# Kernel tuning notes

Hardware: AMD Instinct MI355X
Metric: run time of the kernel (lower is better)

Reference implementation:

```python
import jax, jax.numpy as jnp
import numpy as np

B, C, H, W = 4, 64, 64, 64
DK, DV = 64, 64


def _conv1x1(x, w, b):
    # x: [B,C,H,W], w: [O,C], b: [O] -> [B,O,H,W]
    return jnp.einsum('bchw,oc->bohw', x, w) + b[None, :, None, None]


def _ordered_mask(N, ordering, dtype):
    mask = jnp.tril(jnp.ones((N, N), dtype=dtype))
    if ordering == 1:
        return mask
    elif ordering == 2:
        return jnp.flip(mask, 1)
    elif ordering == 3:
        return jnp.rot90(mask, 1)
    elif ordering == 4:
        return jnp.flip(jnp.rot90(mask, 1), 0)
    elif ordering == 5:
        return jnp.rot90(mask, 2)
    elif ordering == 6:
        return jnp.flip(jnp.rot90(mask, 2), 1)
    elif ordering == 7:
        return jnp.rot90(mask, 3)
    elif ordering == 8:
        return jnp.flip(jnp.rot90(mask, 3), 1)
    return None


def setup_inputs() -> dict:
    key = jax.random.key(0)
    ks = jax.random.split(key, 9)
    s = 0.02
    return {
        'x': jax.random.normal(ks[0], (B, C, H, W), dtype=jnp.float32),
        'Wq': jax.random.normal(ks[1], (DK, C), dtype=jnp.float32) * s,
        'bq': jnp.zeros((DK,), dtype=jnp.float32),
        'Wk': jax.random.normal(ks[2], (DK, C), dtype=jnp.float32) * s,
        'bk': jnp.zeros((DK,), dtype=jnp.float32),
        'Wv': jax.random.normal(ks[3], (DV, C), dtype=jnp.float32) * s,
        'bv': jnp.zeros((DV,), dtype=jnp.float32),
        'Wo': jax.random.normal(ks[4], (DV, DV + C), dtype=jnp.float32) * s,
        'bo': jnp.zeros((DV,), dtype=jnp.float32),
        'ordering': 1,
    }


def reference(x, Wq, bq, Wk, bk, Wv, bv, Wo, bo, ordering):
    b, c, h, w = x.shape
    N = h * w
    dk, dv = Wq.shape[0], Wv.shape[0]
    Q = _conv1x1(x, Wq, bq).reshape(b, dk, N)  # [B,dk,N]
    K = _conv1x1(x, Wk, bk).reshape(b, dk, N)  # [B,dk,N]
    V = _conv1x1(x, Wv, bv).reshape(b, dv, N)  # [B,dv,N]
    logits = jnp.einsum('bdn,bdm->bnm', Q, K)  # [B,N,N] (no 1/sqrt(dk) scaling, matching source)
    weights = jax.nn.softmax(logits, axis=-1)
    m = _ordered_mask(N, ordering, x.dtype)
    if m is not None:
        weights = weights * m  # post-softmax multiplicative mask
    o = jnp.einsum('bnm,bdm->bdn', weights, V).reshape(b, dv, h, w)
    oc = jnp.concatenate([o, x], axis=1)  # [B,dv+C,H,W]
    return _conv1x1(oc, Wo, bo)
```

## Files before the change

kernel.cpp:

```cpp
#include <hip/hip_runtime.h>

typedef __attribute__((ext_vector_type(8))) short short8;
typedef __attribute__((ext_vector_type(4))) short short4v;
typedef __attribute__((ext_vector_type(4))) float f32x4;
typedef __attribute__((ext_vector_type(16))) float f32x16;
typedef __attribute__((ext_vector_type(4))) unsigned int uint4v;
typedef __attribute__((ext_vector_type(2))) unsigned int uint2v;
typedef unsigned short us;
typedef unsigned int u32;

#define NB 4
#define NC 64
#define NN 4096
#define ND 64
#define LOG2E 1.44269504088896340736f

static __device__ __forceinline__ us f2bf(float x) {
    u32 u = __builtin_bit_cast(u32, x);
    u += 0x7FFFu + ((u >> 16) & 1u);
    return (us)(u >> 16);
}

static __device__ __forceinline__ float bf2f(us v) {
    u32 u = ((u32)v) << 16;
    return __builtin_bit_cast(float, u);
}

static __device__ __forceinline__ u32 cvtpk(float a, float b) {
    u32 r;
    asm("v_cvt_pk_bf16_f32 %0, %1, %2" : "=v"(r) : "v"(a), "v"(b));
    return r;
}

static __device__ __forceinline__ short8 comb(short4v a, short4v b) {
    short8 r;
    r[0] = a[0]; r[1] = a[1]; r[2] = a[2]; r[3] = a[3];
    r[4] = b[0]; r[5] = b[1]; r[6] = b[2]; r[7] = b[3];
    return r;
}

static __device__ __forceinline__ void async_copy16(void* lds, const void* g) {
    __builtin_amdgcn_global_load_lds(
        (const __attribute__((address_space(1))) u32*)g,
        (__attribute__((address_space(3))) u32*)lds, 16, 0, 0);
}

static __device__ __forceinline__ int swz8(int row) {
    return (row & 7) ^ ((row >> 3) & 3);
}

__global__ void cvt_kernel(const float* __restrict__ Wo,
                           const float* __restrict__ Wq,
                           const float* __restrict__ Wk,
                           const float* __restrict__ Wv,
                           us* __restrict__ Wob, us* __restrict__ Wqb,
                           us* __restrict__ Wkb, us* __restrict__ Wvb) {
    int i = blockIdx.x * 256 + threadIdx.x;
    if (i < 8192) Wob[i] = f2bf(Wo[i]);
    else if (i < 12288) Wqb[i - 8192] = f2bf(Wq[i - 8192] * LOG2E);
    else if (i < 16384) Wkb[i - 12288] = f2bf(Wk[i - 12288]);
    else if (i < 20480) Wvb[i - 16384] = f2bf(Wv[i - 16384]);
}

__global__ __launch_bounds__(256) void proj_kernel(
    const float* __restrict__ x,
    const us* __restrict__ Wqb, const float* __restrict__ bq,
    const us* __restrict__ Wkb, const float* __restrict__ bk,
    const us* __restrict__ Wvb, const float* __restrict__ bv,
    us* __restrict__ Qt, us* __restrict__ Kt,
    us* __restrict__ Vm, us* __restrict__ Xbt)
{
    __shared__ float xs[64][64];
    __shared__ __align__(16) us xT[64][64];
    const int t = threadIdx.x;
    const int bid = blockIdx.x;
    const int role = bid & 1;
    const int v = bid >> 1;
    const int b = v >> 6;
    const int n0 = (v & 63) << 6;
    const float* xb = x + (size_t)b * NC * NN + n0;
    #pragma unroll
    for (int i = 0; i < 4; ++i) {
        int s = t + i * 256;
        int c = s >> 4, col = (s & 15) << 2;
        *(f32x4*)&xs[c][col] = *(const f32x4*)&xb[(size_t)c * NN + col];
    }
    __syncthreads();
    {
        int n = t & 63, cg = t >> 6;
        int c0 = cg << 4;
        u32 pk[8];
        #pragma unroll
        for (int j = 0; j < 8; ++j) {
            float a0 = xs[c0 + 2 * j][n], a1 = xs[c0 + 2 * j + 1][n];
            pk[j] = (u32)f2bf(a0) | ((u32)f2bf(a1) << 16);
        }
        int b0 = (cg * 2) ^ (n & 7), b1 = (cg * 2 + 1) ^ (n & 7);
        *(uint4v*)&xT[n][b0 * 8] = (uint4v){pk[0], pk[1], pk[2], pk[3]};
        *(uint4v*)&xT[n][b1 * 8] = (uint4v){pk[4], pk[5], pk[6], pk[7]};
        if (role == 1) {
            us* dst = Xbt + (size_t)(b * NN + n0 + n) * ND + c0;
            *(uint4v*)dst       = (uint4v){pk[0], pk[1], pk[2], pk[3]};
            *(uint4v*)(dst + 8) = (uint4v){pk[4], pk[5], pk[6], pk[7]};
        }
    }
    __syncthreads();
    const int w = t >> 6, l = t & 63, h = l >> 4, ln = l & 15;
    const int row = w * 16 + ln;
    short8 xq0 = *(const short8*)&xT[row][((h ^ (row & 7)) << 3)];
    short8 xq1 = *(const short8*)&xT[row][(((4 + h) ^ (row & 7)) << 3)];

    if (role == 0) {
        #pragma unroll
        for (int p = 0; p < 2; ++p) {
            const us* Wb = p ? Wkb : Wqb;
            const float* bias = p ? bk : bq;
            const float sc = p ? 1.0f : LOG2E;
            us* outp = p ? Kt : Qt;
            #pragma unroll
            for (int di = 0; di < 4; ++di) {
                const int d = di * 16 + ln;
                const us* wrb = Wb + (size_t)d * 64;
                short8 a0 = *(const short8*)(wrb + h * 8);
                short8 a1 = *(const short8*)(wrb + 32 + h * 8);
                f32x4 acc = *(const f32x4*)(bias + di * 16 + h * 4);
                acc *= sc;
                acc = __builtin_amdgcn_mfma_f32_16x16x32_bf16(a0, xq0, acc, 0, 0, 0);
                acc = __builtin_amdgcn_mfma_f32_16x16x32_bf16(a1, xq1, acc, 0, 0, 0);
                u32 lo = (u32)f2bf(acc[0]) | ((u32)f2bf(acc[1]) << 16);
                u32 hi2 = (u32)f2bf(acc[2]) | ((u32)f2bf(acc[3]) << 16);
                *(uint2v*)(outp + (size_t)(b * NN + n0 + row) * ND + di * 16 + h * 4) = (uint2v){lo, hi2};
            }
        }
    } else {
        #pragma unroll
        for (int di = 0; di < 4; ++di) {
            const int d = di * 16 + ln;
            const us* wrb = Wvb + (size_t)d * 64;
            short8 a0 = *(const short8*)(wrb + h * 8);
            short8 a1 = *(const short8*)(wrb + 32 + h * 8);
            f32x4 acc = *(const f32x4*)(bv + di * 16 + h * 4);
            acc = __builtin_amdgcn_mfma_f32_16x16x32_bf16(a0, xq0, acc, 0, 0, 0);
            acc = __builtin_amdgcn_mfma_f32_16x16x32_bf16(a1, xq1, acc, 0, 0, 0);
            us* vp = Vm + (size_t)(b * ND + di * 16 + h * 4) * NN + n0 + row;
            vp[0] = f2bf(acc[0]); vp[NN] = f2bf(acc[1]);
            vp[2 * NN] = f2bf(acc[2]); vp[3 * NN] = f2bf(acc[3]);
        }
    }
}

static __device__ __forceinline__ void mask_bounds32(int pt, int n032, int ng,
    int& lo_n, int& hi_n, int& lo_min, int& lo_max, int& hi_min, int& hi_max)
{
    if (pt == 0)      { lo_n = 0;           hi_n = ng;          lo_min = 0;              lo_max = 0;             hi_min = n032;           hi_max = n032 + 31; }
    else if (pt == 1) { lo_n = NN - 1 - ng; hi_n = NN - 1;      lo_min = NN - 32 - n032; lo_max = NN - 1 - n032; hi_min = NN - 1;         hi_max = NN - 1; }
    else if (pt == 2) { lo_n = ng;          hi_n = NN - 1;      lo_min = n032;           lo_max = n032 + 31;     hi_min = NN - 1;         hi_max = NN - 1; }
    else if (pt == 3) { lo_n = 0;           hi_n = NN - 1 - ng; lo_min = 0;              lo_max = 0;             hi_min = NN - 32 - n032; hi_max = NN - 1 - n032; }
    else              { lo_n = 0;           hi_n = NN - 1;      lo_min = 0;              lo_max = 0;             hi_min = NN - 1;         hi_max = NN - 1; }
}

__global__ __launch_bounds__(256, 4) void attn_kernel(
    const us* __restrict__ Qt, const us* __restrict__ Kt,
    const us* __restrict__ Vm,
    const int* __restrict__ ordp,
    us* __restrict__ Opb, float* __restrict__ Lb)
{
    __shared__ __align__(16) us Kl[2][64 * 64];
    __shared__ __align__(16) us Vl[2][64 * 64];

    const int tid = threadIdx.x;
    const int w = tid >> 6, l = tid & 63;
    const int hi = l >> 5, ln = l & 31;
    const int nh = w & 1, mh = (w >> 1) & 1;
    const int bid = blockIdx.x;
    const int vid = (bid & 7) * 128 + (bid >> 3);
    const int b = vid >> 8;
    const int ms = (vid >> 6) & 3;
    const int n0 = (vid & 63) << 6;
    const int mbase = ms << 10;
    const int n032 = n0 + nh * 32;
    const int ng = n032 + ln;

    const int ord = ordp[0];
    int pt = 4;
    if (ord == 1) pt = 0;
    else if (ord == 2 || ord == 3) pt = 1;
    else if (ord == 4 || ord == 5 || ord == 8) pt = 2;
    else if (ord == 6 || ord == 7) pt = 3;
    int lo_n, hi_n, lo_min, lo_max, hi_min, hi_max;
    mask_bounds32(pt, n032, ng, lo_n, hi_n, lo_min, lo_max, hi_min, hi_max);

    int vlo = 0, vhi = NN - 1;
    if (pt == 0)      { vhi = n0 + 63; }
    else if (pt == 1) { vlo = NN - 64 - n0; }
    else if (pt == 2) { vlo = n0; }
    else if (pt == 3) { vhi = NN - 1 - n0; }

    const us* kb = Kt + (size_t)b * NN * ND;
    const us* vb = Vm + (size_t)b * ND * NN;
    const us* qrow = Qt + (size_t)(b * NN + n032 + ln) * ND;
    short8 qf0 = *(const short8*)(qrow + 0 * 16 + hi * 8);
    short8 qf1 = *(const short8*)(qrow + 1 * 16 + hi * 8);
    short8 qf2 = *(const short8*)(qrow + 2 * 16 + hi * 8);
    short8 qf3 = *(const short8*)(qrow + 3 * 16 + hi * 8);

    f32x16 O0, O1, Z;
    #pragma unroll
    for (int i = 0; i < 16; ++i) { O0[i] = 0.f; O1[i] = 0.f; Z[i] = 0.f; }
    float Lp = 0.f;

    auto stage = [&](int buf, int t) {
        const int m_base = mbase + t * 64;
        if (w < 2) {
            #pragma unroll
            for (int r = 0; r < 4; ++r) {
                const int rl = w * 32 + r * 8 + (l >> 3);
                const int blk = l & 7;
                const us* src = kb + (size_t)(m_base + rl) * ND + ((blk ^ swz8(rl)) << 3);
                async_copy16(&Kl[buf][(w * 32 + r * 8) * 64], src);
            }
        } else {
            if (m_base + 63 < vlo || m_base > vhi) return;
            #pragma unroll
            for (int r = 0; r < 4; ++r) {
                const int rl = (w - 2) * 32 + r * 8 + (l >> 3);
                const int blk = l & 7;
                const us* src = vb + (size_t)rl * NN + m_base + ((blk ^ swz8(rl)) << 3);
                async_copy16(&Vl[buf][((w - 2) * 32 + r * 8) * 64], src);
            }
        }
    };

    stage(0, 0);
    for (int t = 0; t < 16; ++t) {
        if (t < 15) {
            stage((t + 1) & 1, t + 1);
            asm volatile("s_waitcnt vmcnt(4)" ::: "memory");
        } else {
            asm volatile("s_waitcnt vmcnt(0)" ::: "memory");
        }
        __builtin_amdgcn_s_barrier();
        __builtin_amdgcn_sched_barrier(0);

        const us* KT = Kl[t & 1];
        const us* VT = Vl[t & 1];
        const int m0s = mbase + t * 64 + mh * 32;
        const bool skip = (m0s + 31 < lo_min) || (m0s > hi_max);
        const bool full = (m0s >= lo_max) && (m0s + 31 <= hi_min);

        __builtin_amdgcn_s_setprio(1);
        {
            const int row = mh * 32 + ln;
            const int rs = swz8(row);
            short8 a0 = *(const short8*)&KT[row * 64 + (((0 + hi) ^ rs) << 3)];
            short8 a1 = *(const short8*)&KT[row * 64 + (((2 + hi) ^ rs) << 3)];
            short8 a2 = *(const short8*)&KT[row * 64 + (((4 + hi) ^ rs) << 3)];
            short8 a3 = *(const short8*)&KT[row * 64 + (((6 + hi) ^ rs) << 3)];
            f32x16 st = __builtin_amdgcn_mfma_f32_32x32x16_bf16(a0, qf0, Z, 0, 0, 0);
            st = __builtin_amdgcn_mfma_f32_32x32x16_bf16(a1, qf1, st, 0, 0, 0);
            st = __builtin_amdgcn_mfma_f32_32x32x16_bf16(a2, qf2, st, 0, 0, 0);
            st = __builtin_amdgcn_mfma_f32_32x32x16_bf16(a3, qf3, st, 0, 0, 0);

            float p[16];
            float lp0 = 0.f, lp1 = 0.f;
            #pragma unroll
            for (int r = 0; r < 16; ++r) {
                p[r] = __builtin_amdgcn_exp2f(st[r]);
                if (r & 1) lp1 += p[r]; else lp0 += p[r];
            }
            Lp += lp0 + lp1;
            if (!skip) {
                if (!full) {
                    #pragma unroll
                    for (int r = 0; r < 16; ++r) {
                        const int mg = m0s + (r & 3) + 8 * (r >> 2) + 4 * hi;
                        if (mg < lo_n || mg > hi_n) p[r] = 0.f;
                    }
                }
                #pragma unroll
                for (int c16 = 0; c16 < 2; ++c16) {
                    uint4v pw;
                    pw[0] = cvtpk(p[c16 * 8 + 0], p[c16 * 8 + 1]);
                    pw[1] = cvtpk(p[c16 * 8 + 2], p[c16 * 8 + 3]);
                    pw[2] = cvtpk(p[c16 * 8 + 4], p[c16 * 8 + 5]);
                    pw[3] = cvtpk(p[c16 * 8 + 6], p[c16 * 8 + 7]);
                    short8 pb = __builtin_bit_cast(short8, pw);
                    const int blkA = mh * 4 + c16 * 2;
                    {
                        const int rv = ln, rvs = swz8(rv);
                        short4v va  = *(const short4v*)&VT[rv * 64 + ((blkA ^ rvs) << 3) + hi * 4];
                        short4v vb2 = *(const short4v*)&VT[rv * 64 + (((blkA + 1) ^ rvs) << 3) + hi * 4];
                        O0 = __builtin_amdgcn_mfma_f32_32x32x16_bf16(comb(va, vb2), pb, O0, 0, 0, 0);
                    }
                    {
                        const int rv = 32 + ln, rvs = swz8(rv);
                        short4v va  = *(const short4v*)&VT[rv * 64 + ((blkA ^ rvs) << 3) + hi * 4];
                        short4v vb2 = *(const short4v*)&VT[rv * 64 + (((blkA + 1) ^ rvs) << 3) + hi * 4];
                        O1 = __builtin_amdgcn_mfma_f32_32x32x16_bf16(comb(va, vb2), pb, O1, 0, 0, 0);
                    }
                }
            }
        }
        __builtin_amdgcn_s_setprio(0);
        __builtin_amdgcn_sched_barrier(0);
        __builtin_amdgcn_s_barrier();
    }

    float Lw = Lp + __shfl_xor(Lp, 32);

    float* cO = (float*)&Kl[0][0];
    float* cL = (float*)&Vl[0][0];
    if (mh == 1) {
        float* dsto = cO + nh * 2048 + ln * 64;
        #pragma unroll
        for (int rq = 0; rq < 4; ++rq) {
            f32x4 s0, s1;
            #pragma unroll
            for (int j = 0; j < 4; ++j) { s0[j] = O0[rq * 4 + j]; s1[j] = O1[rq * 4 + j]; }
            *(f32x4*)&dsto[rq * 8 + hi * 4] = s0;
            *(f32x4*)&dsto[32 + rq * 8 + hi * 4] = s1;
        }
        if (hi == 0) cL[nh * 32 + ln] = Lw;
    }
    __syncthreads();
    if (mh == 1) return;

    const float gL = Lw + cL[nh * 32 + ln];
    const float* sp = cO + nh * 2048 + ln * 64;
    f32x16 On0 = O0, On1 = O1;
    #pragma unroll
    for (int rq = 0; rq < 4; ++rq) {
        f32x4 a = *(const f32x4*)&sp[rq * 8 + hi * 4];
        f32x4 c = *(const f32x4*)&sp[32 + rq * 8 + hi * 4];
        #pragma unroll
        for (int j = 0; j < 4; ++j) { On0[rq * 4 + j] += a[j]; On1[rq * 4 + j] += c[j]; }
    }

    us* opb = Opb + ((size_t)(ms * NB + b) * 64) * NN;
    #pragma unroll
    for (int r = 0; r < 16; ++r) {
        const int d0 = (r & 3) + 8 * (r >> 2) + 4 * hi;
        opb[(size_t)d0 * NN + n032 + ln] = f2bf(On0[r]);
        opb[(size_t)(d0 + 32) * NN + n032 + ln] = f2bf(On1[r]);
    }
    if (hi == 0) Lb[(size_t)(ms * NB + b) * NN + n032 + ln] = gL;
}

__global__ __launch_bounds__(256) void combine_kernel(
    const us* __restrict__ Opb, const float* __restrict__ Lb,
    const us* __restrict__ Xbt, const us* __restrict__ Wob,
    const float* __restrict__ bo, float* __restrict__ out)
{
    const int t = threadIdx.x;
    const int w = t >> 6, l = t & 63, hi = l >> 5, ln = l & 31;
    const int gw = blockIdx.x * 4 + w;
    const int b = gw >> 7;
    const int n032 = (gw & 127) << 5;
    const int q = n032 + ln;

    f32x16 On0, On1;
    #pragma unroll
    for (int r = 0; r < 16; ++r) {
        const int d0 = (r & 3) + 8 * (r >> 2) + 4 * hi;
        float s0 = 0.f, s1 = 0.f;
        #pragma unroll
        for (int i = 0; i < 4; ++i) {
            const us* opb = Opb + ((size_t)(i * NB + b) * 64) * NN;
            s0 += bf2f(opb[(size_t)d0 * NN + q]);
            s1 += bf2f(opb[(size_t)(d0 + 32) * NN + q]);
        }
        On0[r] = s0; On1[r] = s1;
    }
    float gL = 0.f;
    #pragma unroll
    for (int i = 0; i < 4; ++i) gL += Lb[(size_t)(i * NB + b) * NN + q];
    const float rl2 = 1.0f / gL;
    #pragma unroll
    for (int i = 0; i < 16; ++i) { On0[i] *= rl2; On1[i] *= rl2; }

    short8 Bf[8];
    {
        uint4v w0, w1, w2, w3;
        w0[0] = cvtpk(On0[0], On0[1]);   w0[1] = cvtpk(On0[2], On0[3]);
        w0[2] = cvtpk(On0[4], On0[5]);   w0[3] = cvtpk(On0[6], On0[7]);
        w1[0] = cvtpk(On0[8], On0[9]);   w1[1] = cvtpk(On0[10], On0[11]);
        w1[2] = cvtpk(On0[12], On0[13]); w1[3] = cvtpk(On0[14], On0[15]);
        w2[0] = cvtpk(On1[0], On1[1]);   w2[1] = cvtpk(On1[2], On1[3]);
        w2[2] = cvtpk(On1[4], On1[5]);   w2[3] = cvtpk(On1[6], On1[7]);
        w3[0] = cvtpk(On1[8], On1[9]);   w3[1] = cvtpk(On1[10], On1[11]);
        w3[2] = cvtpk(On1[12], On1[13]); w3[3] = cvtpk(On1[14], On1[15]);
        Bf[0] = __builtin_bit_cast(short8, w0);
        Bf[1] = __builtin_bit_cast(short8, w1);
        Bf[2] = __builtin_bit_cast(short8, w2);
        Bf[3] = __builtin_bit_cast(short8, w3);
    }
    const us* xrow = Xbt + (size_t)(b * NN + q) * ND;
    #pragma unroll
    for (int c4 = 0; c4 < 4; ++c4)
        Bf[4 + c4] = comb(*(const short4v*)(xrow + c4 * 16 + hi * 4),
                          *(const short4v*)(xrow + c4 * 16 + hi * 4 + 8));

    f32x16 acc0, acc1;
    #pragma unroll
    for (int rq = 0; rq < 4; ++rq) {
        f32x4 b0 = *(const f32x4*)&bo[rq * 8 + hi * 4];
        f32x4 b1 = *(const f32x4*)&bo[32 + rq * 8 + hi * 4];
        #pragma unroll
        for (int j = 0; j < 4; ++j) { acc0[rq * 4 + j] = b0[j]; acc1[rq * 4 + j] = b1[j]; }
    }
    const us* wr0 = Wob + (size_t)ln * 128;
    const us* wr1 = Wob + (size_t)(32 + ln) * 128;
    #pragma unroll
    for (int kc = 0; kc < 8; ++kc) {
        short8 wf0 = comb(*(const short4v*)(wr0 + kc * 16 + hi * 4),
                          *(const short4v*)(wr0 + kc * 16 + hi * 4 + 8));
        short8 wf1 = comb(*(const short4v*)(wr1 + kc * 16 + hi * 4),
                          *(const short4v*)(wr1 + kc * 16 + hi * 4 + 8));
        acc0 = __builtin_amdgcn_mfma_f32_32x32x16_bf16(wf0, Bf[kc], acc0, 0, 0, 0);
        acc1 = __builtin_amdgcn_mfma_f32_32x32x16_bf16(wf1, Bf[kc], acc1, 0, 0, 0);
    }
    #pragma unroll
    for (int r = 0; r < 16; ++r) {
        const int od = (r & 3) + 8 * (r >> 2) + 4 * hi;
        out[((size_t)b * 64 + od) * NN + q] = acc0[r];
        out[((size_t)b * 64 + 32 + od) * NN + q] = acc1[r];
    }
}

extern "C" void kernel_launch(void* const* d_in, const int* in_sizes, int n_in,
                              void* d_out, int out_size, void* d_ws, size_t ws_size,
                              hipStream_t stream) {
    (void)in_sizes; (void)n_in; (void)out_size; (void)ws_size;
    const float* x  = (const float*)d_in[0];
    const float* Wq = (const float*)d_in[1];
    const float* bq = (const float*)d_in[2];
    const float* Wk = (const float*)d_in[3];
    const float* bk = (const float*)d_in[4];
    const float* Wv = (const float*)d_in[5];
    const float* bv = (const float*)d_in[6];
    const float* Wo = (const float*)d_in[7];
    const float* bo = (const float*)d_in[8];
    const int* ord  = (const int*)d_in[9];
    float* out = (float*)d_out;

    us* Qt  = (us*)d_ws;
    us* Kt  = Qt  + (size_t)NB * NN * ND;
    us* Vm  = Kt  + (size_t)NB * NN * ND;
    us* Xbt = Vm  + (size_t)NB * NN * ND;
    us* Wob = Xbt + (size_t)NB * NN * ND;
    us* Opb = Wob + ND * (ND + NC);
    float* Lb = (float*)(Opb + (size_t)4 * NB * 64 * NN);
    us* Wqb = (us*)(Lb + (size_t)4 * NB * NN);
    us* Wkb = Wqb + 4096;
    us* Wvb = Wkb + 4096;

    cvt_kernel<<<dim3(80), dim3(256), 0, stream>>>(Wo, Wq, Wk, Wv, Wob, Wqb, Wkb, Wvb);
    proj_kernel<<<dim3(NB * 64 * 2), dim3(256), 0, stream>>>(
        x, Wqb, bq, Wkb, bk, Wvb, bv, Qt, Kt, Vm, Xbt);
    attn_kernel<<<dim3(1024), dim3(256), 0, stream>>>(Qt, Kt, Vm, ord, Opb, Lb);
    combine_kernel<<<dim3(128), dim3(256), 0, stream>>>(Opb, Lb, Xbt, Wob, bo, out);
}
```

Measured before the change: 56.50 us.

## Triple-buffer K/V staging, pack partial outputs as bf16 pairs, shrink combine blocks

The attention kernel moves from double to triple LDS buffering, prefetching two tiles ahead and dropping the trailing per-iteration barrier. It also removes the V-load skip for masked tiles and lowers the occupancy hint from 4 to 3 blocks per SM. Partial outputs are now written as packed bf16 pairs (u32) for wider stores and loads, and the combine kernel runs 512 single-wave blocks instead of 128 four-wave blocks. The aim is to hide global-load latency and cut store and load transaction counts, at the cost of more LDS, lower occupancy and extra V traffic on masked tiles.

```diff
diff --git a/kernel.cpp b/kernel.cpp
--- a/kernel.cpp
+++ b/kernel.cpp
@@ -159,14 +159,14 @@
     else              { lo_n = 0;           hi_n = NN - 1;      lo_min = 0;              lo_max = 0;             hi_min = NN - 1;         hi_max = NN - 1; }
 }
 
-__global__ __launch_bounds__(256, 4) void attn_kernel(
+__global__ __launch_bounds__(256, 3) void attn_kernel(
     const us* __restrict__ Qt, const us* __restrict__ Kt,
     const us* __restrict__ Vm,
     const int* __restrict__ ordp,
-    us* __restrict__ Opb, float* __restrict__ Lb)
+    u32* __restrict__ Opk, float* __restrict__ Lb)
 {
-    __shared__ __align__(16) us Kl[2][64 * 64];
-    __shared__ __align__(16) us Vl[2][64 * 64];
+    __shared__ __align__(16) us Kl[3][64 * 64];
+    __shared__ __align__(16) us Vl[3][64 * 64];
 
     const int tid = threadIdx.x;
     const int w = tid >> 6, l = tid & 63;
@@ -190,12 +190,6 @@
     int lo_n, hi_n, lo_min, lo_max, hi_min, hi_max;
     mask_bounds32(pt, n032, ng, lo_n, hi_n, lo_min, lo_max, hi_min, hi_max);
 
-    int vlo = 0, vhi = NN - 1;
-    if (pt == 0)      { vhi = n0 + 63; }
-    else if (pt == 1) { vlo = NN - 64 - n0; }
-    else if (pt == 2) { vlo = n0; }
-    else if (pt == 3) { vhi = NN - 1 - n0; }
-
     const us* kb = Kt + (size_t)b * NN * ND;
     const us* vb = Vm + (size_t)b * ND * NN;
     const us* qrow = Qt + (size_t)(b * NN + n032 + ln) * ND;
@@ -220,7 +214,6 @@
                 async_copy16(&Kl[buf][(w * 32 + r * 8) * 64], src);
             }
         } else {
-            if (m_base + 63 < vlo || m_base > vhi) return;
             #pragma unroll
             for (int r = 0; r < 4; ++r) {
                 const int rl = (w - 2) * 32 + r * 8 + (l >> 3);
@@ -232,9 +225,12 @@
     };
 
     stage(0, 0);
+    stage(1, 1);
     for (int t = 0; t < 16; ++t) {
-        if (t < 15) {
-            stage((t + 1) & 1, t + 1);
+        if (t < 14) {
+            stage((t + 2) % 3, t + 2);
+            asm volatile("s_waitcnt vmcnt(8)" ::: "memory");
+        } else if (t == 14) {
             asm volatile("s_waitcnt vmcnt(4)" ::: "memory");
         } else {
             asm volatile("s_waitcnt vmcnt(0)" ::: "memory");
@@ -242,8 +238,9 @@
         __builtin_amdgcn_s_barrier();
         __builtin_amdgcn_sched_barrier(0);
 
-        const us* KT = Kl[t & 1];
-        const us* VT = Vl[t & 1];
+        const int bc = t % 3;
+        const us* KT = Kl[bc];
+        const us* VT = Vl[bc];
         const int m0s = mbase + t * 64 + mh * 32;
         const bool skip = (m0s + 31 < lo_min) || (m0s > hi_max);
         const bool full = (m0s >= lo_max) && (m0s + 31 <= hi_min);
@@ -303,9 +300,9 @@
         }
         __builtin_amdgcn_s_setprio(0);
         __builtin_amdgcn_sched_barrier(0);
-        __builtin_amdgcn_s_barrier();
-    }
-
+    }
+
+    __syncthreads();
     float Lw = Lp + __shfl_xor(Lp, 32);
 
     float* cO = (float*)&Kl[0][0];
@@ -336,40 +333,43 @@
         for (int j = 0; j < 4; ++j) { On0[rq * 4 + j] += a[j]; On1[rq * 4 + j] += c[j]; }
     }
 
-    us* opb = Opb + ((size_t)(ms * NB + b) * 64) * NN;
-    #pragma unroll
-    for (int r = 0; r < 16; ++r) {
-        const int d0 = (r & 3) + 8 * (r >> 2) + 4 * hi;
-        opb[(size_t)d0 * NN + n032 + ln] = f2bf(On0[r]);
-        opb[(size_t)(d0 + 32) * NN + n032 + ln] = f2bf(On1[r]);
-    }
-    if (hi == 0) Lb[(size_t)(ms * NB + b) * NN + n032 + ln] = gL;
-}
-
-__global__ __launch_bounds__(256) void combine_kernel(
-    const us* __restrict__ Opb, const float* __restrict__ Lb,
+    u32* opk = Opk + ((size_t)(ms * NB + b) * 32) * NN + n032 + ln;
+    #pragma unroll
+    for (int rp = 0; rp < 16; rp += 2) {
+        const int dp = ((rp & 3) >> 1) + 4 * (rp >> 2) + 2 * hi;
+        opk[(size_t)dp * NN] = cvtpk(On0[rp], On0[rp + 1]);
+        opk[(size_t)(dp + 16) * NN] = cvtpk(On1[rp], On1[rp + 1]);
+    }
+    if (hi == 0) Lb[(size_t)(ms * NB + b) * NN + n032 + ln] = Lw + cL[nh * 32 + ln];
+}
+
+__global__ __launch_bounds__(64) void combine_kernel(
+    const u32* __restrict__ Opk, const float* __restrict__ Lb,
     const us* __restrict__ Xbt, const us* __restrict__ Wob,
     const float* __restrict__ bo, float* __restrict__ out)
 {
-    const int t = threadIdx.x;
-    const int w = t >> 6, l = t & 63, hi = l >> 5, ln = l & 31;
-    const int gw = blockIdx.x * 4 + w;
+    const int l = threadIdx.x, hi = l >> 5, ln = l & 31;
+    const int gw = blockIdx.x;
     const int b = gw >> 7;
     const int n032 = (gw & 127) << 5;
     const int q = n032 + ln;
 
     f32x16 On0, On1;
     #pragma unroll
-    for (int r = 0; r < 16; ++r) {
-        const int d0 = (r & 3) + 8 * (r >> 2) + 4 * hi;
-        float s0 = 0.f, s1 = 0.f;
-        #pragma unroll
-        for (int i = 0; i < 4; ++i) {
-            const us* opb = Opb + ((size_t)(i * NB + b) * 64) * NN;
-            s0 += bf2f(opb[(size_t)d0 * NN + q]);
-            s1 += bf2f(opb[(size_t)(d0 + 32) * NN + q]);
-        }
-        On0[r] = s0; On1[r] = s1;
+    for (int i = 0; i < 16; ++i) { On0[i] = 0.f; On1[i] = 0.f; }
+    #pragma unroll
+    for (int part = 0; part < 4; ++part) {
+        const u32* pb = Opk + ((size_t)(part * NB + b) * 32) * NN + q;
+        #pragma unroll
+        for (int rp = 0; rp < 16; rp += 2) {
+            const int dp = ((rp & 3) >> 1) + 4 * (rp >> 2) + 2 * hi;
+            u32 w0 = pb[(size_t)dp * NN];
+            u32 w1 = pb[(size_t)(dp + 16) * NN];
+            On0[rp]     += bf2f((us)(w0 & 0xFFFFu));
+            On0[rp + 1] += bf2f((us)(w0 >> 16));
+            On1[rp]     += bf2f((us)(w1 & 0xFFFFu));
+            On1[rp + 1] += bf2f((us)(w1 >> 16));
+        }
     }
     float gL = 0.f;
     #pragma unroll
@@ -448,8 +448,8 @@
     us* Vm  = Kt  + (size_t)NB * NN * ND;
     us* Xbt = Vm  + (size_t)NB * NN * ND;
     us* Wob = Xbt + (size_t)NB * NN * ND;
-    us* Opb = Wob + ND * (ND + NC);
-    float* Lb = (float*)(Opb + (size_t)4 * NB * 64 * NN);
+    u32* Opk = (u32*)(Wob + ND * (ND + NC));
+    float* Lb = (float*)(Opk + (size_t)16 * 32 * NN);
     us* Wqb = (us*)(Lb + (size_t)4 * NB * NN);
     us* Wkb = Wqb + 4096;
     us* Wvb = Wkb + 4096;
@@ -457,6 +457,6 @@
     cvt_kernel<<<dim3(80), dim3(256), 0, stream>>>(Wo, Wq, Wk, Wv, Wob, Wqb, Wkb, Wvb);
     proj_kernel<<<dim3(NB * 64 * 2), dim3(256), 0, stream>>>(
         x, Wqb, bq, Wkb, bk, Wvb, bv, Qt, Kt, Vm, Xbt);
-    attn_kernel<<<dim3(1024), dim3(256), 0, stream>>>(Qt, Kt, Vm, ord, Opb, Lb);
-    combine_kernel<<<dim3(128), dim3(256), 0, stream>>>(Opb, Lb, Xbt, Wob, bo, out);
-}
+    attn_kernel<<<dim3(1024), dim3(256), 0, stream>>>(Qt, Kt, Vm, ord, Opk, Lb);
+    combine_kernel<<<dim3(512), dim3(64), 0, stream>>>(Opk, Lb, Xbt, Wob, bo, out);
+}
```

Result: slower. 59.03 us (+4.5%).
